# Kernel tuning notes

Hardware: AMD Instinct MI355X
Metric: run time of the kernel (lower is better)

The kernel has to match this reference:

```python
import jax, jax.numpy as jnp
import numpy as np

HEADS, DIM_HEAD, CHUNK, GROUPS, EPS = 4, 32, 2048, 8, 1e-5


def setup_inputs() -> dict:
    key = jax.random.key(0)
    ks = jax.random.split(key, 10)
    B, C, H, W = 1, 128, 128, 128
    inner = HEADS * DIM_HEAD  # 128
    s = 0.02
    return {
        "x": jax.random.normal(ks[0], (B, C, H, W), jnp.float32),
        "w_qkv": jax.random.normal(ks[1], (3 * inner, C), jnp.float32) * s,
        "se_w1": jax.random.normal(ks[2], (inner // 4, inner), jnp.float32) * s,
        "se_b1": jax.random.normal(ks[3], (inner // 4,), jnp.float32) * s,
        "se_w2": jax.random.normal(ks[4], (inner, inner // 4), jnp.float32) * s,
        "se_b2": jax.random.normal(ks[5], (inner,), jnp.float32) * s,
        "out_w": jax.random.normal(ks[6], (C, inner), jnp.float32) * s,
        "out_b": jax.random.normal(ks[7], (C,), jnp.float32) * s,
        "gn_w": 1.0 + jax.random.normal(ks[8], (C,), jnp.float32) * s,
        "gn_b": jax.random.normal(ks[9], (C,), jnp.float32) * s,
    }


def reference(x, w_qkv, se_w1, se_b1, se_w2, se_b2, out_w, out_b, gn_w, gn_b):
    B, C, H, W = x.shape
    inner = HEADS * DIM_HEAD
    hw = H * W
    nc = hw // CHUNK  # hw chosen divisible by CHUNK
    scale = DIM_HEAD ** -0.5

    # 1x1 conv to qkv (no bias)
    qkv = jnp.einsum('oc,bchw->bohw', w_qkv, x)  # [B, 3*inner, H, W]
    q, k, v = jnp.split(qkv.reshape(B, 3 * inner, hw), 3, axis=1)

    def to_blocks(t):  # [B, inner, hw] -> [B*heads, dh, nc, CHUNK]
        return t.reshape(B * HEADS, DIM_HEAD, nc, CHUNK)

    q, k, v = to_blocks(q), to_blocks(k), to_blocks(v)

    # block-diagonal attention: attn[n, j] = softmax_j(q[:, n]^T k[:, j])
    attn = jax.nn.softmax(jnp.einsum('bdnc,bdne->bnce', q, k) * scale, axis=-1)
    # chunk_out[d, j] = sum_c v[d, c] * attn[c, j]  (contracts the un-normalized axis, as in torch bmm(v, attn))
    out = jnp.einsum('bdnc,bncj->bdnj', v, attn).reshape(B, inner, H, W)

    # SE gating
    s = out.mean(axis=(2, 3))                       # [B, inner]
    s = jax.nn.silu(s @ se_w1.T + se_b1)            # [B, inner//4]
    g = jax.nn.sigmoid(s @ se_w2.T + se_b2)         # [B, inner]
    out = out * g[:, :, None, None]

    # output 1x1 conv + GroupNorm(8, C)
    y = jnp.einsum('oc,bchw->bohw', out_w, out) + out_b[None, :, None, None]
    yg = y.reshape(B, GROUPS, C // GROUPS, H, W)
    mu = yg.mean(axis=(2, 3, 4), keepdims=True)
    var = yg.var(axis=(2, 3, 4), keepdims=True)
    yn = ((yg - mu) * jax.lax.rsqrt(var + EPS)).reshape(B, C, H, W)
    return yn * gn_w[None, :, None, None] + gn_b[None, :, None, None]
```

## Files before the change

### kernel.cpp

```cpp
#include <hip/hip_runtime.h>
#include <hip/hip_bf16.h>

#define HW 16384
#define QSCALE (0.17677669529663687f * 1.4426950408889634f)

typedef __attribute__((ext_vector_type(8))) short short8;
typedef __attribute__((ext_vector_type(4))) float floatx4;
typedef __attribute__((ext_vector_type(16))) float floatx16;

__device__ inline unsigned cvt_pk_bf16(float a, float b) {
  unsigned r;
  asm("v_cvt_pk_bf16_f32 %0, %1, %2" : "=v"(r) : "v"(a), "v"(b));
  return r;
}
__device__ inline unsigned short f2bf(float a) {
  return (unsigned short)(cvt_pk_bf16(a, 0.f) & 0xffff);
}
__device__ inline float bf2f(unsigned short u) {
  union { unsigned u; float f; } c;
  c.u = (unsigned)u << 16;
  return c.f;
}
__device__ inline void permlane32_swap(unsigned& a, unsigned& b) {
  asm("v_permlane32_swap_b32 %0, %1" : "+v"(a), "+v"(b));
}
__device__ inline float fast_exp2(float x) {
  return __builtin_amdgcn_exp2f(x);
}

__global__ __launch_bounds__(256) void cast_w(
    const float* __restrict__ w, unsigned short* __restrict__ w_bf) {
  const int i4 = (blockIdx.x * 256 + threadIdx.x) * 4;
  const int o = i4 >> 7;
  const float sc = (o < 128) ? QSCALE : 1.f;
  float4 v = *(const float4*)&w[i4];
  uint2 u = {cvt_pk_bf16(v.x * sc, v.y * sc), cvt_pk_bf16(v.z * sc, v.w * sc)};
  *(uint2*)&w_bf[i4] = u;
}

__global__ __launch_bounds__(256) void cast_transpose_x(
    const float* __restrict__ x, unsigned short* __restrict__ x_t) {
  __shared__ float tile[128][65];
  const int p0 = blockIdx.x * 64;
  const int t = threadIdx.x;
  #pragma unroll
  for (int i = 0; i < 32; ++i) {
    int idx = t + i * 256;
    int c = idx >> 6, p = idx & 63;
    tile[c][p] = x[c * HW + p0 + p];
  }
  __syncthreads();
  const int p = t >> 2, q = t & 3;
  unsigned u[16];
  #pragma unroll
  for (int i = 0; i < 16; ++i)
    u[i] = cvt_pk_bf16(tile[q * 32 + 2 * i][p], tile[q * 32 + 2 * i + 1][p]);
  unsigned short* dst = &x_t[(p0 + p) * 128 + q * 32];
  #pragma unroll
  for (int i = 0; i < 4; ++i) *(uint4*)&dst[i * 8] = *(const uint4*)&u[i * 4];
}

__global__ __launch_bounds__(512) void gemm_qkv(
    const unsigned short* __restrict__ w_bf, const unsigned short* __restrict__ x_t,
    unsigned short* __restrict__ q_t, unsigned short* __restrict__ k_t,
    unsigned short* __restrict__ v_bf) {
  const int wave = threadIdx.x >> 6, lane = threadIdx.x & 63;
  const int lr = lane & 15, g = lane >> 4;
  const int p0 = blockIdx.x * 64;
  const int ow = wave * 48;
  const floatx4 zero = {0.f, 0.f, 0.f, 0.f};

  short8 a[3][4];
  #pragma unroll
  for (int mf = 0; mf < 3; ++mf)
    #pragma unroll
    for (int kk = 0; kk < 4; ++kk)
      a[mf][kk] = *(const short8*)&w_bf[(ow + mf * 16 + lr) * 128 + kk * 32 + g * 8];

  floatx4 acc[3][4];
  #pragma unroll
  for (int mf = 0; mf < 3; ++mf)
    #pragma unroll
    for (int nf = 0; nf < 4; ++nf) acc[mf][nf] = zero;

  #pragma unroll
  for (int kk = 0; kk < 4; ++kk) {
    #pragma unroll
    for (int nf = 0; nf < 4; ++nf) {
      short8 b = *(const short8*)&x_t[(p0 + nf * 16 + lr) * 128 + kk * 32 + g * 8];
      #pragma unroll
      for (int mf = 0; mf < 3; ++mf)
        acc[mf][nf] = __builtin_amdgcn_mfma_f32_16x16x32_bf16(a[mf][kk], b, acc[mf][nf], 0, 0, 0);
    }
  }

  #pragma unroll
  for (int mf = 0; mf < 3; ++mf) {
    const int ob = ow + mf * 16;
    #pragma unroll
    for (int nf = 0; nf < 4; ++nf) {
      const int p = p0 + nf * 16 + lr;
      const int c = p & 2047, nn = p >> 11;
      floatx4 r = acc[mf][nf];
      if (ob < 128) {
        const int bh = ob >> 5, d0 = (ob & 31) + g * 4;
        uint2 u = {cvt_pk_bf16(r[0], r[1]), cvt_pk_bf16(r[2], r[3])};
        *(uint2*)&q_t[((bh * 8 + nn) * 2048 + c) * 32 + d0] = u;
      } else if (ob < 256) {
        const int oo = ob - 128, bh = oo >> 5, d0 = (oo & 31) + g * 4;
        uint2 u = {cvt_pk_bf16(r[0], r[1]), cvt_pk_bf16(r[2], r[3])};
        *(uint2*)&k_t[((bh * 8 + nn) * 2048 + c) * 32 + d0] = u;
      } else {
        const int d = ob - 256 + g * 4;
        #pragma unroll
        for (int rr = 0; rr < 4; ++rr) v_bf[(d + rr) * HW + p] = f2bf(r[rr]);
      }
    }
  }
}

__global__ __launch_bounds__(256) void row_mean_v(
    const unsigned short* __restrict__ v_bf, float* __restrict__ s) {
  const int ch = blockIdx.x;
  float sum = 0;
  for (int i = threadIdx.x; i < 2048; i += 256) {
    short8 u = *(const short8*)&v_bf[ch * HW + i * 8];
    #pragma unroll
    for (int k = 0; k < 8; ++k) sum += bf2f((unsigned short)u[k]);
  }
  __shared__ float red[256];
  red[threadIdx.x] = sum;
  __syncthreads();
  for (int st = 128; st > 0; st >>= 1) {
    if (threadIdx.x < st) red[threadIdx.x] += red[threadIdx.x + st];
    __syncthreads();
  }
  if (threadIdx.x == 0) s[ch] = red[0] * (1.f / HW);
}

__global__ __launch_bounds__(128) void se_mlp(
    const float* __restrict__ s, const float* __restrict__ w1,
    const float* __restrict__ b1, const float* __restrict__ w2,
    const float* __restrict__ b2, const float* __restrict__ out_w,
    unsigned short* __restrict__ w_g) {
  __shared__ float s_sh[128], s1_sh[32], g_sh[128];
  const int t = threadIdx.x;
  s_sh[t] = s[t];
  __syncthreads();
  if (t < 32) {
    float a = b1[t];
    for (int c = 0; c < 128; ++c) a += w1[t * 128 + c] * s_sh[c];
    s1_sh[t] = a / (1.f + __expf(-a));
  }
  __syncthreads();
  {
    float a = b2[t];
    for (int i = 0; i < 32; ++i) a += w2[t * 32 + i] * s1_sh[i];
    g_sh[t] = 1.f / (1.f + __expf(-a));
  }
  __syncthreads();
  for (int o = 0; o < 128; ++o) w_g[o * 128 + t] = f2bf(out_w[o * 128 + t] * g_sh[t]);
}

__global__ __launch_bounds__(256, 4) void attn_stats_mfma(
    const unsigned short* __restrict__ q_t, const unsigned short* __restrict__ k_t,
    float* __restrict__ zpart) {
  const int wave = threadIdx.x >> 6, lane = threadIdx.x & 63;
  const int f = blockIdx.x;
  const int bn = ((f >> 7) & 3) * 8 + (f & 7);
  const int ct = (f >> 3) & 15;
  const int epart = f >> 9;
  const int l31 = lane & 31, h = lane >> 5;
  const int c0 = ct * 128 + wave * 32;
  const floatx16 z16 = {0.f,0.f,0.f,0.f,0.f,0.f,0.f,0.f,
                        0.f,0.f,0.f,0.f,0.f,0.f,0.f,0.f};

  const unsigned short* qp = &q_t[(bn * 2048 + c0 + l31) * 32 + h * 8];
  short8 aq0 = *(const short8*)qp;
  short8 aq1 = *(const short8*)(qp + 16);

  float z[16] = {};
  const unsigned short* kb = &k_t[(bn * 2048 + epart * 512 + l31) * 32 + h * 8];

  short8 b0a = *(const short8*)&kb[0];
  short8 b0b = *(const short8*)&kb[16];
  short8 b1a = *(const short8*)&kb[32 * 32];
  short8 b1b = *(const short8*)&kb[32 * 32 + 16];

  for (int e0 = 0; e0 < 512; e0 += 64) {
    const unsigned short* nk = &kb[(e0 + 64) * 32];
    short8 nb0a = *(const short8*)&nk[0];
    short8 nb0b = *(const short8*)&nk[16];
    short8 nb1a = *(const short8*)&nk[32 * 32];
    short8 nb1b = *(const short8*)&nk[32 * 32 + 16];

    floatx16 s1 = __builtin_amdgcn_mfma_f32_32x32x16_bf16(aq0, b0a, z16, 0, 0, 0);
    s1 = __builtin_amdgcn_mfma_f32_32x32x16_bf16(aq1, b0b, s1, 0, 0, 0);
    floatx16 s2 = __builtin_amdgcn_mfma_f32_32x32x16_bf16(aq0, b1a, z16, 0, 0, 0);
    s2 = __builtin_amdgcn_mfma_f32_32x32x16_bf16(aq1, b1b, s2, 0, 0, 0);
    #pragma unroll
    for (int r = 0; r < 16; ++r) z[r] += fast_exp2(s1[r]) + fast_exp2(s2[r]);

    b0a = nb0a; b0b = nb0b; b1a = nb1a; b1b = nb1b;
  }
  #pragma unroll
  for (int r = 0; r < 16; ++r) {
    float v = z[r];
    v += __shfl_xor(v, 1); v += __shfl_xor(v, 2); v += __shfl_xor(v, 4);
    v += __shfl_xor(v, 8); v += __shfl_xor(v, 16);
    z[r] = v;
  }
  if (l31 == 0) {
    #pragma unroll
    for (int r = 0; r < 16; ++r)
      zpart[epart * 65536 + bn * 2048 + c0 + (r & 3) + 8 * (r >> 2) + 4 * h] = z[r];
  }
}

__global__ __launch_bounds__(256) void vz_cast(
    const unsigned short* __restrict__ v_bf, const float* __restrict__ zpart,
    unsigned short* __restrict__ vz) {
  const int idx = (blockIdx.x * 256 + threadIdx.x) * 8;
  const int row = idx >> 14, p = idx & 16383;
  const int bh = row >> 5, nn = p >> 11, c = p & 2047;
  short8 v8 = *(const short8*)&v_bf[idx];
  const int zb = (bh * 8 + nn) * 2048 + c;
  float zs[8];
  #pragma unroll
  for (int i = 0; i < 8; ++i)
    zs[i] = __builtin_amdgcn_rcpf((zpart[zb + i] + zpart[65536 + zb + i]) +
                                  (zpart[131072 + zb + i] + zpart[196608 + zb + i]));
  unsigned u[4];
  #pragma unroll
  for (int i = 0; i < 4; ++i)
    u[i] = cvt_pk_bf16(bf2f((unsigned short)v8[2 * i]) * zs[2 * i],
                       bf2f((unsigned short)v8[2 * i + 1]) * zs[2 * i + 1]);
  uint4 o = {u[0], u[1], u[2], u[3]};
  *(uint4*)&vz[idx] = o;
}

__global__ __launch_bounds__(256, 4) void attn_apply_mfma(
    const unsigned short* __restrict__ q_t, const unsigned short* __restrict__ k_t,
    const unsigned short* __restrict__ vz, unsigned short* __restrict__ att_t) {
  const int wave = threadIdx.x >> 6, lane = threadIdx.x & 63;
  const int f = blockIdx.x;
  const int bn = ((f >> 6) & 3) * 8 + (f & 7);
  const int jg = (f >> 3) & 7;
  const int cpart = f >> 8;
  const int bh = bn >> 3, nn = bn & 7;
  const int jA = jg * 256 + wave * 64;
  const int jB = jA + 32;
  const int l31 = lane & 31, h = lane >> 5;
  const floatx16 z16 = {0.f,0.f,0.f,0.f,0.f,0.f,0.f,0.f,
                        0.f,0.f,0.f,0.f,0.f,0.f,0.f,0.f};

  const unsigned short* kpA = &k_t[(bn * 2048 + jA + l31) * 32 + h * 8];
  const unsigned short* kpB = &k_t[(bn * 2048 + jB + l31) * 32 + h * 8];
  short8 bkA0 = *(const short8*)kpA, bkA1 = *(const short8*)(kpA + 16);
  short8 bkB0 = *(const short8*)kpB, bkB1 = *(const short8*)(kpB + 16);

  floatx16 accA = z16, accB = z16;
  const unsigned short* qb = &q_t[(bn * 2048 + cpart * 512 + l31) * 32 + h * 8];
  const unsigned short* vb = &vz[(bh * 32 + l31) * HW + nn * 2048 + cpart * 512 + h * 8];

  short8 aq0 = *(const short8*)&qb[0];
  short8 aq1 = *(const short8*)&qb[16];
  short8 av0 = *(const short8*)&vb[0];
  short8 av1 = *(const short8*)&vb[16];

  for (int c0 = 0; c0 < 512; c0 += 32) {
    short8 naq0 = *(const short8*)&qb[(c0 + 32) * 32];
    short8 naq1 = *(const short8*)&qb[(c0 + 32) * 32 + 16];
    short8 nav0 = *(const short8*)&vb[c0 + 32];
    short8 nav1 = *(const short8*)&vb[c0 + 48];

    {
      floatx16 s = __builtin_amdgcn_mfma_f32_32x32x16_bf16(aq0, bkA0, z16, 0, 0, 0);
      s = __builtin_amdgcn_mfma_f32_32x32x16_bf16(aq1, bkA1, s, 0, 0, 0);
      unsigned pk0 = cvt_pk_bf16(fast_exp2(s[0]),  fast_exp2(s[1]));
      unsigned pk1 = cvt_pk_bf16(fast_exp2(s[2]),  fast_exp2(s[3]));
      unsigned pk2 = cvt_pk_bf16(fast_exp2(s[4]),  fast_exp2(s[5]));
      unsigned pk3 = cvt_pk_bf16(fast_exp2(s[6]),  fast_exp2(s[7]));
      unsigned pk4 = cvt_pk_bf16(fast_exp2(s[8]),  fast_exp2(s[9]));
      unsigned pk5 = cvt_pk_bf16(fast_exp2(s[10]), fast_exp2(s[11]));
      unsigned pk6 = cvt_pk_bf16(fast_exp2(s[12]), fast_exp2(s[13]));
      unsigned pk7 = cvt_pk_bf16(fast_exp2(s[14]), fast_exp2(s[15]));
      permlane32_swap(pk0, pk2);
      permlane32_swap(pk1, pk3);
      permlane32_swap(pk4, pk6);
      permlane32_swap(pk5, pk7);
      union { uint4 u; short8 s8; } b0, b1;
      b0.u = make_uint4(pk0, pk1, pk2, pk3);
      b1.u = make_uint4(pk4, pk5, pk6, pk7);
      accA = __builtin_amdgcn_mfma_f32_32x32x16_bf16(av0, b0.s8, accA, 0, 0, 0);
      accA = __builtin_amdgcn_mfma_f32_32x32x16_bf16(av1, b1.s8, accA, 0, 0, 0);
    }
    {
      floatx16 s = __builtin_amdgcn_mfma_f32_32x32x16_bf16(aq0, bkB0, z16, 0, 0, 0);
      s = __builtin_amdgcn_mfma_f32_32x32x16_bf16(aq1, bkB1, s, 0, 0, 0);
      unsigned pk0 = cvt_pk_bf16(fast_exp2(s[0]),  fast_exp2(s[1]));
      unsigned pk1 = cvt_pk_bf16(fast_exp2(s[2]),  fast_exp2(s[3]));
      unsigned pk2 = cvt_pk_bf16(fast_exp2(s[4]),  fast_exp2(s[5]));
      unsigned pk3 = cvt_pk_bf16(fast_exp2(s[6]),  fast_exp2(s[7]));
      unsigned pk4 = cvt_pk_bf16(fast_exp2(s[8]),  fast_exp2(s[9]));
      unsigned pk5 = cvt_pk_bf16(fast_exp2(s[10]), fast_exp2(s[11]));
      unsigned pk6 = cvt_pk_bf16(fast_exp2(s[12]), fast_exp2(s[13]));
      unsigned pk7 = cvt_pk_bf16(fast_exp2(s[14]), fast_exp2(s[15]));
      permlane32_swap(pk0, pk2);
      permlane32_swap(pk1, pk3);
      permlane32_swap(pk4, pk6);
      permlane32_swap(pk5, pk7);
      union { uint4 u; short8 s8; } b0, b1;
      b0.u = make_uint4(pk0, pk1, pk2, pk3);
      b1.u = make_uint4(pk4, pk5, pk6, pk7);
      accB = __builtin_amdgcn_mfma_f32_32x32x16_bf16(av0, b0.s8, accB, 0, 0, 0);
      accB = __builtin_amdgcn_mfma_f32_32x32x16_bf16(av1, b1.s8, accB, 0, 0, 0);
    }
    aq0 = naq0; aq1 = naq1; av0 = nav0; av1 = nav1;
  }

  unsigned short* orowA = att_t + cpart * 2097152 +
                          (nn * 2048 + jA + l31) * 128 + bh * 32 + 4 * h;
  unsigned short* orowB = att_t + cpart * 2097152 +
                          (nn * 2048 + jB + l31) * 128 + bh * 32 + 4 * h;
  #pragma unroll
  for (int q = 0; q < 4; ++q) {
    uint2 uA = {cvt_pk_bf16(accA[4 * q], accA[4 * q + 1]),
                cvt_pk_bf16(accA[4 * q + 2], accA[4 * q + 3])};
    *(uint2*)&orowA[q * 8] = uA;
    uint2 uB = {cvt_pk_bf16(accB[4 * q], accB[4 * q + 1]),
                cvt_pk_bf16(accB[4 * q + 2], accB[4 * q + 3])};
    *(uint2*)&orowB[q * 8] = uB;
  }
}

__global__ __launch_bounds__(256) void gemm_out(
    const unsigned short* __restrict__ w_g, const unsigned short* __restrict__ att_t,
    const float* __restrict__ out_b, unsigned short* __restrict__ ybuf_bf,
    float* __restrict__ part) {
  const int wave = threadIdx.x >> 6, lane = threadIdx.x & 63;
  const int lr = lane & 15, g = lane >> 4;
  const int p0 = blockIdx.x * 64;
  const int o0 = wave * 32;
  const floatx4 zero = {0.f, 0.f, 0.f, 0.f};

  short8 a[2][4];
  #pragma unroll
  for (int mf = 0; mf < 2; ++mf)
    #pragma unroll
    for (int kk = 0; kk < 4; ++kk)
      a[mf][kk] = *(const short8*)&w_g[(o0 + mf * 16 + lr) * 128 + kk * 32 + g * 8];

  floatx4 acc[2][4];
  #pragma unroll
  for (int mf = 0; mf < 2; ++mf)
    #pragma unroll
    for (int nf = 0; nf < 4; ++nf) acc[mf][nf] = zero;

  #pragma unroll
  for (int ks = 0; ks < 16; ++ks) {
    const unsigned short* att = att_t + (ks >> 2) * 2097152;
    const int kk = ks & 3;
    #pragma unroll
    for (int nf = 0; nf < 4; ++nf) {
      short8 b = *(const short8*)&att[(p0 + nf * 16 + lr) * 128 + kk * 32 + g * 8];
      acc[0][nf] = __builtin_amdgcn_mfma_f32_16x16x32_bf16(a[0][kk], b, acc[0][nf], 0, 0, 0);
      acc[1][nf] = __builtin_amdgcn_mfma_f32_16x16x32_bf16(a[1][kk], b, acc[1][nf], 0, 0, 0);
    }
  }

  float sg[2] = {0.f, 0.f}, ssg[2] = {0.f, 0.f};
  #pragma unroll
  for (int mf = 0; mf < 2; ++mf) {
    #pragma unroll
    for (int nf = 0; nf < 4; ++nf) {
      #pragma unroll
      for (int r = 0; r < 4; ++r) {
        const int o = o0 + mf * 16 + g * 4 + r;
        float y = acc[mf][nf][r] + out_b[o];
        ybuf_bf[o * HW + p0 + nf * 16 + lr] = f2bf(y);
        sg[mf] += y;
        ssg[mf] += y * y;
      }
    }
  }
  #pragma unroll
  for (int mf = 0; mf < 2; ++mf) {
    float a1 = sg[mf], a2 = ssg[mf];
    #pragma unroll
    for (int st = 1; st < 64; st <<= 1) {
      a1 += __shfl_xor(a1, st);
      a2 += __shfl_xor(a2, st);
    }
    if (lane == 0) {
      part[(blockIdx.x * 8 + wave * 2 + mf) * 2 + 0] = a1;
      part[(blockIdx.x * 8 + wave * 2 + mf) * 2 + 1] = a2;
    }
  }
}

__global__ __launch_bounds__(256) void gn_finalize(
    const float* __restrict__ part, float* __restrict__ stat) {
  const int gg = blockIdx.x;
  const int t = threadIdx.x;
  __shared__ float r1[256], r2[256];
  r1[t] = part[(t * 8 + gg) * 2 + 0];
  r2[t] = part[(t * 8 + gg) * 2 + 1];
  __syncthreads();
  for (int st = 128; st > 0; st >>= 1) {
    if (t < st) { r1[t] += r1[t + st]; r2[t] += r2[t + st]; }
    __syncthreads();
  }
  if (t == 0) {
    const float inv_n = 1.f / (16.f * HW);
    float mu = r1[0] * inv_n;
    float var = r2[0] * inv_n - mu * mu;
    stat[gg * 2 + 0] = mu;
    stat[gg * 2 + 1] = rsqrtf(var + 1e-5f);
  }
}

__global__ __launch_bounds__(256) void gn_apply(
    const unsigned short* __restrict__ ybuf_bf, const float* __restrict__ stat,
    const float* __restrict__ gn_w, const float* __restrict__ gn_b,
    float* __restrict__ outp) {
  const int i = (blockIdx.x * 256 + threadIdx.x) * 8;
  const int ch = i >> 14;
  const int g = ch >> 4;
  float mu = stat[g * 2], rs = stat[g * 2 + 1];
  float w = gn_w[ch] * rs;
  float b = gn_b[ch] - mu * w;
  short8 v = *(const short8*)&ybuf_bf[i];
  float4 r0 = {bf2f((unsigned short)v[0]) * w + b, bf2f((unsigned short)v[1]) * w + b,
               bf2f((unsigned short)v[2]) * w + b, bf2f((unsigned short)v[3]) * w + b};
  float4 r1 = {bf2f((unsigned short)v[4]) * w + b, bf2f((unsigned short)v[5]) * w + b,
               bf2f((unsigned short)v[6]) * w + b, bf2f((unsigned short)v[7]) * w + b};
  *(float4*)&outp[i] = r0;
  *(float4*)&outp[i + 4] = r1;
}

extern "C" void kernel_launch(void* const* d_in, const int* in_sizes, int n_in,
                              void* d_out, int out_size, void* d_ws, size_t ws_size,
                              hipStream_t stream) {
  const float* x     = (const float*)d_in[0];
  const float* w_qkv = (const float*)d_in[1];
  const float* se_w1 = (const float*)d_in[2];
  const float* se_b1 = (const float*)d_in[3];
  const float* se_w2 = (const float*)d_in[4];
  const float* se_b2 = (const float*)d_in[5];
  const float* out_w = (const float*)d_in[6];
  const float* out_b = (const float*)d_in[7];
  const float* gn_w  = (const float*)d_in[8];
  const float* gn_b  = (const float*)d_in[9];
  float* out = (float*)d_out;

  float* ws = (float*)d_ws;
  float* zpart = ws;
  float* se_s  = zpart + 262144;
  float* part  = se_s + 128;
  float* stat  = part + 4096;
  unsigned short* w_bf    = (unsigned short*)(stat + 16);
  unsigned short* x_t     = w_bf + 49152;
  unsigned short* q_t     = x_t + 2097152;
  unsigned short* k_t     = q_t + 2097152;
  unsigned short* v_bf    = k_t + 2097152;
  unsigned short* vz      = v_bf + 2097152;
  unsigned short* w_g     = vz + 2097152;
  unsigned short* att_t   = w_g + 16384;
  unsigned short* ybuf_bf = att_t + 8388608;

  cast_w<<<48, 256, 0, stream>>>(w_qkv, w_bf);
  cast_transpose_x<<<256, 256, 0, stream>>>(x, x_t);
  gemm_qkv<<<256, 512, 0, stream>>>(w_bf, x_t, q_t, k_t, v_bf);
  row_mean_v<<<128, 256, 0, stream>>>(v_bf, se_s);
  se_mlp<<<1, 128, 0, stream>>>(se_s, se_w1, se_b1, se_w2, se_b2, out_w, w_g);
  attn_stats_mfma<<<2048, 256, 0, stream>>>(q_t, k_t, zpart);
  vz_cast<<<1024, 256, 0, stream>>>(v_bf, zpart, vz);
  attn_apply_mfma<<<1024, 256, 0, stream>>>(q_t, k_t, vz, att_t);
  gemm_out<<<256, 256, 0, stream>>>(w_g, att_t, out_b, ybuf_bf, part);
  gn_finalize<<<8, 256, 0, stream>>>(part, stat);
  gn_apply<<<1024, 256, 0, stream>>>(ybuf_bf, stat, gn_w, gn_b, out);
}
```

Measured before the change: 113.8 us.

## Fuse weight/x casts and fold V row-mean into QKV GEMM epilogue

Merges the weight cast and the x cast-transpose into one launch, with the extra blocks handling the weights. It also drops the separate row_mean_v kernel: gemm_qkv now writes per-block partial sums of V from fp32 accumulators, and se_mlp reduces those 256 partials. This saves two kernel launches and a full re-read of v_bf. In exchange se_mlp runs a serial 256-step reduction in a single block, and the SE mean is now taken from the fp32 accumulators rather than the bf16-rounded V, so it can differ slightly from before.

```diff
diff --git a/kernel.cpp b/kernel.cpp
--- a/kernel.cpp
+++ b/kernel.cpp
@@ -28,21 +28,21 @@
   return __builtin_amdgcn_exp2f(x);
 }
 
-__global__ __launch_bounds__(256) void cast_w(
-    const float* __restrict__ w, unsigned short* __restrict__ w_bf) {
-  const int i4 = (blockIdx.x * 256 + threadIdx.x) * 4;
-  const int o = i4 >> 7;
-  const float sc = (o < 128) ? QSCALE : 1.f;
-  float4 v = *(const float4*)&w[i4];
-  uint2 u = {cvt_pk_bf16(v.x * sc, v.y * sc), cvt_pk_bf16(v.z * sc, v.w * sc)};
-  *(uint2*)&w_bf[i4] = u;
-}
-
-__global__ __launch_bounds__(256) void cast_transpose_x(
-    const float* __restrict__ x, unsigned short* __restrict__ x_t) {
+__global__ __launch_bounds__(256) void cast_wx(
+    const float* __restrict__ w, const float* __restrict__ x,
+    unsigned short* __restrict__ w_bf, unsigned short* __restrict__ x_t) {
   __shared__ float tile[128][65];
+  const int t = threadIdx.x;
+  if (blockIdx.x >= 256) {
+    const int i4 = ((blockIdx.x - 256) * 256 + t) * 4;
+    const int o = i4 >> 7;
+    const float sc = (o < 128) ? QSCALE : 1.f;
+    float4 v = *(const float4*)&w[i4];
+    uint2 u = {cvt_pk_bf16(v.x * sc, v.y * sc), cvt_pk_bf16(v.z * sc, v.w * sc)};
+    *(uint2*)&w_bf[i4] = u;
+    return;
+  }
   const int p0 = blockIdx.x * 64;
-  const int t = threadIdx.x;
   #pragma unroll
   for (int i = 0; i < 32; ++i) {
     int idx = t + i * 256;
@@ -63,7 +63,7 @@
 __global__ __launch_bounds__(512) void gemm_qkv(
     const unsigned short* __restrict__ w_bf, const unsigned short* __restrict__ x_t,
     unsigned short* __restrict__ q_t, unsigned short* __restrict__ k_t,
-    unsigned short* __restrict__ v_bf) {
+    unsigned short* __restrict__ v_bf, float* __restrict__ part_v) {
   const int wave = threadIdx.x >> 6, lane = threadIdx.x & 63;
   const int lr = lane & 15, g = lane >> 4;
   const int p0 = blockIdx.x * 64;
@@ -93,6 +93,12 @@
         acc[mf][nf] = __builtin_amdgcn_mfma_f32_16x16x32_bf16(a[mf][kk], b, acc[mf][nf], 0, 0, 0);
     }
   }
+
+  float vsum[3][4];
+  #pragma unroll
+  for (int mf = 0; mf < 3; ++mf)
+    #pragma unroll
+    for (int rr = 0; rr < 4; ++rr) vsum[mf][rr] = 0.f;
 
   #pragma unroll
   for (int mf = 0; mf < 3; ++mf) {
@@ -113,39 +119,39 @@
       } else {
         const int d = ob - 256 + g * 4;
         #pragma unroll
-        for (int rr = 0; rr < 4; ++rr) v_bf[(d + rr) * HW + p] = f2bf(r[rr]);
+        for (int rr = 0; rr < 4; ++rr) {
+          v_bf[(d + rr) * HW + p] = f2bf(r[rr]);
+          vsum[mf][rr] += r[rr];
+        }
       }
     }
   }
-}
-
-__global__ __launch_bounds__(256) void row_mean_v(
-    const unsigned short* __restrict__ v_bf, float* __restrict__ s) {
-  const int ch = blockIdx.x;
-  float sum = 0;
-  for (int i = threadIdx.x; i < 2048; i += 256) {
-    short8 u = *(const short8*)&v_bf[ch * HW + i * 8];
-    #pragma unroll
-    for (int k = 0; k < 8; ++k) sum += bf2f((unsigned short)u[k]);
-  }
-  __shared__ float red[256];
-  red[threadIdx.x] = sum;
-  __syncthreads();
-  for (int st = 128; st > 0; st >>= 1) {
-    if (threadIdx.x < st) red[threadIdx.x] += red[threadIdx.x + st];
-    __syncthreads();
-  }
-  if (threadIdx.x == 0) s[ch] = red[0] * (1.f / HW);
+  #pragma unroll
+  for (int mf = 0; mf < 3; ++mf) {
+    const int ob = ow + mf * 16;
+    if (ob >= 256) {
+      #pragma unroll
+      for (int rr = 0; rr < 4; ++rr) {
+        float vv = vsum[mf][rr];
+        vv += __shfl_xor(vv, 1); vv += __shfl_xor(vv, 2);
+        vv += __shfl_xor(vv, 4); vv += __shfl_xor(vv, 8);
+        if (lr == 0)
+          part_v[blockIdx.x * 128 + (ob - 256) + g * 4 + rr] = vv;
+      }
+    }
+  }
 }
 
 __global__ __launch_bounds__(128) void se_mlp(
-    const float* __restrict__ s, const float* __restrict__ w1,
+    const float* __restrict__ part_v, const float* __restrict__ w1,
     const float* __restrict__ b1, const float* __restrict__ w2,
     const float* __restrict__ b2, const float* __restrict__ out_w,
     unsigned short* __restrict__ w_g) {
   __shared__ float s_sh[128], s1_sh[32], g_sh[128];
   const int t = threadIdx.x;
-  s_sh[t] = s[t];
+  float a0 = 0.f;
+  for (int b = 0; b < 256; ++b) a0 += part_v[b * 128 + t];
+  s_sh[t] = a0 * (1.f / HW);
   __syncthreads();
   if (t < 32) {
     float a = b1[t];
@@ -455,10 +461,10 @@
   float* out = (float*)d_out;
 
   float* ws = (float*)d_ws;
-  float* zpart = ws;
-  float* se_s  = zpart + 262144;
-  float* part  = se_s + 128;
-  float* stat  = part + 4096;
+  float* zpart  = ws;
+  float* part_v = zpart + 262144;
+  float* part   = part_v + 32768;
+  float* stat   = part + 4096;
   unsigned short* w_bf    = (unsigned short*)(stat + 16);
   unsigned short* x_t     = w_bf + 49152;
   unsigned short* q_t     = x_t + 2097152;
@@ -469,11 +475,9 @@
   unsigned short* att_t   = w_g + 16384;
   unsigned short* ybuf_bf = att_t + 8388608;
 
-  cast_w<<<48, 256, 0, stream>>>(w_qkv, w_bf);
-  cast_transpose_x<<<256, 256, 0, stream>>>(x, x_t);
-  gemm_qkv<<<256, 512, 0, stream>>>(w_bf, x_t, q_t, k_t, v_bf);
-  row_mean_v<<<128, 256, 0, stream>>>(v_bf, se_s);
-  se_mlp<<<1, 128, 0, stream>>>(se_s, se_w1, se_b1, se_w2, se_b2, out_w, w_g);
+  cast_wx<<<304, 256, 0, stream>>>(w_qkv, x, w_bf, x_t);
+  gemm_qkv<<<256, 512, 0, stream>>>(w_bf, x_t, q_t, k_t, v_bf, part_v);
+  se_mlp<<<1, 128, 0, stream>>>(part_v, se_w1, se_b1, se_w2, se_b2, out_w, w_g);
   attn_stats_mfma<<<2048, 256, 0, stream>>>(q_t, k_t, zpart);
   vz_cast<<<1024, 256, 0, stream>>>(v_bf, zpart, vz);
   attn_apply_mfma<<<1024, 256, 0, stream>>>(q_t, k_t, vz, att_t);
```

New measurement: 110.9 us. 2.5% less time.
